# Kernel tuning notes

Measured on AMD Instinct MI355X. Metric: run time of the kernel, lower is better.

Reference implementation:

```python
import jax, jax.numpy as jnp
import numpy as np

B, V, H, W = 1, 88, 128, 256
P = 2                  # patch size
D = 128                # hidden_dim = embed_dim // latent_ratio = 1536 // 12
NG = 12                # n_group (== latent_ratio)
NH = 2                 # heads per attention = num_heads // latent_ratio = 24 // 12
E = NG * D             # embed_dim = 1536
HD = D // NH
SCALE = HD ** -0.5

# Static ragged group index sets derived from the variable names (sizes 7,7,7,7,7,9,9,9,9,9,17,6).
# Pressure-level vars are ordered z,q,t,u,v per level; levels [50..400]=7 levels, [50..600]=9 levels.
_off = {'z': 0, 'q': 1, 't': 2, 'u': 3, 'v': 4}
GROUPS = []
for name in ['u1', 'v1', 't1', 'q1', 'z1', 'u2', 'v2', 't2', 'q2', 'z2', 'surf', 'const']:
    if name[-1] in '12':
        nl = 7 if name[-1] == '1' else 9
        GROUPS.append(np.array([5 * li + _off[name[0]] for li in range(nl)]))
    elif name == 'surf':
        GROUPS.append(np.arange(65, 82))   # 17 surface vars
    else:
        GROUPS.append(np.arange(82, 88))   # 6 constant vars


def setup_inputs() -> dict:
    key = jax.random.key(0)
    ks = jax.random.split(key, 16)
    return {
        "x": jax.random.normal(ks[0], (B, V, H, W), jnp.float32),
        # per-variable conv patch-embed weights, flattened to (V, P*P, D)
        "conv_w": jax.random.normal(ks[1], (V, P * P, D), jnp.float32) * 0.05,
        "conv_b": jax.random.normal(ks[2], (V, D), jnp.float32) * 0.02,
        "channel_embed": jax.random.normal(ks[3], (1, V, D), jnp.float32) * 0.02,
        "channel_query": jax.random.uniform(ks[4], (1, NG, D), jnp.float32) * 0.2,
        # 12 distinct MultiheadAttention modules: packed in_proj (3D, D) + out_proj
        "grp_in_w": jax.random.normal(ks[5], (NG, 3 * D, D), jnp.float32) * 0.05,
        "grp_in_b": jax.random.normal(ks[6], (NG, 3 * D), jnp.float32) * 0.02,
        "grp_out_w": jax.random.normal(ks[7], (NG, D, D), jnp.float32) * 0.05,
        "grp_out_b": jax.random.normal(ks[8], (NG, D), jnp.float32) * 0.02,
        "ens_query": jax.random.uniform(ks[9], (1, NG, D), jnp.float32) * 0.2,
        "ens_in_w": jax.random.normal(ks[10], (3 * D, D), jnp.float32) * 0.05,
        "ens_in_b": jax.random.normal(ks[11], (3 * D,), jnp.float32) * 0.02,
        "ens_out_w": jax.random.normal(ks[12], (D, D), jnp.float32) * 0.05,
        "ens_out_b": jax.random.normal(ks[13], (D,), jnp.float32) * 0.02,
        "ln_gamma": jnp.ones((E,), jnp.float32),
        "ln_beta": jnp.zeros((E,), jnp.float32),
    }


def reference(x, conv_w, conv_b, channel_embed, channel_query,
              grp_in_w, grp_in_b, grp_out_w, grp_out_b,
              ens_query, ens_in_w, ens_in_b, ens_out_w, ens_out_b,
              ln_gamma, ln_beta):
    b, v, h, w = x.shape
    hp, wp = h // P, w // P
    L = hp * wp
    # non-overlapping stride-P conv with 1 input channel == patchify + per-variable matmul
    patches = x.reshape(b, v, hp, P, wp, P).transpose(0, 1, 2, 4, 3, 5).reshape(b, v, L, P * P)
    xe = jnp.einsum('bvlp,vpd->bvld', patches, conv_w) + conv_b[None, :, None, :]
    xe = xe + channel_embed[:, :, None, :]                 # (B, V, L, D)
    xn = xe.transpose(0, 2, 1, 3).reshape(b * L, v, D)     # (N, V, D), N = B*L

    outs = []
    for i, ids in enumerate(GROUPS):                       # 12 fixed, structurally distinct groups
        kv = xn[:, ids, :]                                 # (N, g, D), ragged g
        Wq, Wk, Wv = grp_in_w[i, :D], grp_in_w[i, D:2 * D], grp_in_w[i, 2 * D:]
        bq, bk, bv = grp_in_b[i, :D], grp_in_b[i, D:2 * D], grp_in_b[i, 2 * D:]
        q = (channel_query[0, i] @ Wq.T + bq).reshape(NH, HD)
        k = (kv @ Wk.T + bk).reshape(-1, len(ids), NH, HD)
        vv = (kv @ Wv.T + bv).reshape(-1, len(ids), NH, HD)
        a = jax.nn.softmax(jnp.einsum('hd,nghd->nhg', q, k) * SCALE, axis=-1)
        o = jnp.einsum('nhg,nghd->nhd', a, vv).reshape(-1, D)
        outs.append(o @ grp_out_w[i].T + grp_out_b[i])
    out = jnp.stack(outs, axis=1)                          # (N, 12, D)

    Wq, Wk, Wv = ens_in_w[:D], ens_in_w[D:2 * D], ens_in_w[2 * D:]
    bq, bk, bv = ens_in_b[:D], ens_in_b[D:2 * D], ens_in_b[2 * D:]
    q = (ens_query[0] @ Wq.T + bq).reshape(NG, NH, HD)     # 12 ensemble query tokens
    k = (out @ Wk.T + bk).reshape(-1, NG, NH, HD)
    vv = (out @ Wv.T + bv).reshape(-1, NG, NH, HD)
    a = jax.nn.softmax(jnp.einsum('thd,nshd->nhts', q, k) * SCALE, axis=-1)
    r = jnp.einsum('nhts,nshd->nthd', a, vv).reshape(-1, NG, D)
    r = (r @ ens_out_w.T + ens_out_b).reshape(b, L, E)     # (B, L, embed_dim)

    mu = r.mean(axis=-1, keepdims=True)
    var = r.var(axis=-1, keepdims=True)
    return (r - mu) * jax.lax.rsqrt(var + 1e-5) * ln_gamma + ln_beta
```

## Files before the change

kernel.cpp:

```cpp
#include <hip/hip_runtime.h>


typedef __attribute__((ext_vector_type(8))) short short8;
typedef __attribute__((ext_vector_type(4))) float f32x4;

__constant__ int GOFF[13] = {0,7,14,21,28,35,44,53,62,71,80,97,103};
__constant__ int K5A[12]  = {35,35,35,35,35,45,45,45,45,45,85,30};
__constant__ int SLOTS3[12] = {3,3,3,3,3,3,3,3,3,3,6,2};
__constant__ int FOFFA[12] = {0,3,6,9,12,15,18,21,24,27,30,36};
__constant__ int GSLOT[103] = {
  3,8,13,18,23,28,33,
  4,9,14,19,24,29,34,
  2,7,12,17,22,27,32,
  1,6,11,16,21,26,31,
  0,5,10,15,20,25,30,
  3,8,13,18,23,28,33,38,43,
  4,9,14,19,24,29,34,39,44,
  2,7,12,17,22,27,32,37,42,
  1,6,11,16,21,26,31,36,41,
  0,5,10,15,20,25,30,35,40,
  45,46,47,48,49,50,51,52,53,54,55,56,57,58,59,60,61,
  62,63,64,65,66,67};
__constant__ int GIDX[103] = {
  0,0,0,0,0,0,0, 1,1,1,1,1,1,1, 2,2,2,2,2,2,2, 3,3,3,3,3,3,3, 4,4,4,4,4,4,4,
  5,5,5,5,5,5,5,5,5, 6,6,6,6,6,6,6,6,6, 7,7,7,7,7,7,7,7,7, 8,8,8,8,8,8,8,8,8,
  9,9,9,9,9,9,9,9,9,
  10,10,10,10,10,10,10,10,10,10,10,10,10,10,10,10,10,
  11,11,11,11,11,11};
__constant__ int TGI[38] = {0,0,0,1,1,1,2,2,2,3,3,3,4,4,4,5,5,5,6,6,6,7,7,7,
                            8,8,8,9,9,9,10,10,10,10,10,10,11,11};
__constant__ int TNT[38] = {0,1,2,0,1,2,0,1,2,0,1,2,0,1,2,0,1,2,0,1,2,0,1,2,
                            0,1,2,0,1,2,0,1,2,3,4,5,0,1};

constexpr int cSLOTS[12] = {3,3,3,3,3,3,3,3,3,3,6,2};
constexpr int cFOFFA[12] = {0,3,6,9,12,15,18,21,24,27,30,36};
constexpr int cK5[12]    = {35,35,35,35,35,45,45,45,45,45,85,30};
constexpr int cGOFFC[12] = {0,7,14,21,28,35,44,53,62,71,80,97};
constexpr int cC0[12]    = {3,4,2,1,0,3,4,2,1,0,45,62};
constexpr int cSTP[12]   = {5,5,5,5,5,5,5,5,5,5,1,1};

#define QK_GRP 0
#define QK_ENS 3072
#define QB_GRP 6144
#define QB_ENS 6176
#define CGRP   6208
#define CENS   7744
#define CWQ_BYTE   43776
#define MPL_BYTE   50432
#define CW2_BYTE   836864
#define MEB_BYTE   1623296
#define QKEB_BYTE  1688832
#define FWS_BYTE   1697024

__device__ __forceinline__ float bf2f(unsigned short s) {
  return __uint_as_float(((unsigned)s) << 16);
}
__device__ __forceinline__ unsigned short f2bf(float f) {
  unsigned u = __float_as_uint(f);
  u += 0x7fffu + ((u >> 16) & 1u);
  return (unsigned short)(u >> 16);
}

__global__ void hwe_p1(const float* __restrict__ giw, const float* __restrict__ gib,
                       const float* __restrict__ gow, const float* __restrict__ gob,
                       const float* __restrict__ cq,  const float* __restrict__ eq,
                       const float* __restrict__ eiw, const float* __restrict__ eib,
                       const float* __restrict__ eow, const float* __restrict__ eob,
                       const float* __restrict__ cw,  const float* __restrict__ cb,
                       const float* __restrict__ ce,
                       float* __restrict__ wsf, unsigned short* __restrict__ MA,
                       unsigned short* __restrict__ CW2,
                       unsigned short* __restrict__ MeB, unsigned short* __restrict__ Fws) {
  int blk = blockIdx.x, tid = threadIdx.x;
  int wave = tid >> 6, lane = tid & 63;
  if (blk < 48) {
    __shared__ float qf[64];
    bool ens = blk >= 24;
    int bi = ens ? blk - 24 : blk;
    int i = bi >> 1, h = bi & 1;
    const float* W  = ens ? eiw : giw + i*49152;
    const float* bv = ens ? eib : gib + i*384;
    const float* qv = ens ? eq + i*128 : cq + i*128;
    for (int it = 0; it < 16; ++it) {
      int dp = it*4 + wave;
      const float* wrow = W + (h*64 + dp)*128;
      float acc = wrow[lane]*qv[lane] + wrow[lane+64]*qv[lane+64];
#pragma unroll
      for (int off = 32; off > 0; off >>= 1) acc += __shfl_down(acc, off);
      if (lane == 0) qf[dp] = acc + bv[h*64 + dp];
    }
    __syncthreads();
    if (tid < 128) {
      int e = tid;
      const float* Wk = W + (128 + h*64)*128 + e;
      float a0=0.f,a1=0.f,a2=0.f,a3=0.f;
      for (int dp = 0; dp < 64; dp += 4) {
        a0 += qf[dp+0] * Wk[(dp+0)*128];
        a1 += qf[dp+1] * Wk[(dp+1)*128];
        a2 += qf[dp+2] * Wk[(dp+2)*128];
        a3 += qf[dp+3] * Wk[(dp+3)*128];
      }
      wsf[(ens ? QK_ENS : QK_GRP) + bi*128 + e] = (a0+a1)+(a2+a3);
    }
    if (wave == 3) {
      float acc = qf[lane] * bv[128 + h*64 + lane];
#pragma unroll
      for (int off = 32; off > 0; off >>= 1) acc += __shfl_down(acc, off);
      if (lane == 0) wsf[(ens ? QB_ENS : QB_GRP) + bi] = acc;
    }
  } else if (blk < 1584) {
    int b2 = blk - 48;
    int gi = b2 >> 7, r = b2 & 127;
    int ep = tid, h = ep >> 7, e = ep & 127;
    const float* wo = gow + gi*16384 + r*128 + h*64;
    const float* wv = giw + gi*49152 + (256 + h*64)*128 + e;
    float a0=0.f,a1=0.f,a2=0.f,a3=0.f;
    for (int hd = 0; hd < 64; hd += 4) {
      a0 += wo[hd+0] * wv[(hd+0)*128];
      a1 += wo[hd+1] * wv[(hd+1)*128];
      a2 += wo[hd+2] * wv[(hd+2)*128];
      a3 += wo[hd+3] * wv[(hd+3)*128];
    }
    float acc = (a0+a1)+(a2+a3);
    int mt = r >> 4, lr = r & 15, kt = e >> 5, q = (e >> 3) & 3, j = e & 7;
    MA[(((gi*2 + h)*8 + mt)*4 + kt)*512 + (q*16 + lr)*8 + j] = f2bf(acc);
  } else if (blk < 1712) {
    int f2 = (blk - 1584)*256 + tid;
    int r = f2 >> 8, ep = f2 & 255;
    int h = ep >> 7, e = ep & 127;
    const float* wo = eow + r*128 + h*64;
    const float* wv = eiw + (256 + h*64)*128 + e;
    float a0=0.f,a1=0.f,a2=0.f,a3=0.f;
    for (int hd = 0; hd < 64; hd += 4) {
      a0 += wo[hd+0] * wv[(hd+0)*128];
      a1 += wo[hd+1] * wv[(hd+1)*128];
      a2 += wo[hd+2] * wv[(hd+2)*128];
      a3 += wo[hd+3] * wv[(hd+3)*128];
    }
    float acc = (a0+a1)+(a2+a3);
    int mt = r >> 4, lr = r & 15, kt = ep >> 5, q = (ep >> 3) & 3, j = ep & 7;
    MeB[((mt*8 + kt)*64 + (q*16 + lr))*8 + j] = f2bf(acc);
  } else if (blk < 2096) {
    int id = (blk - 1712)*4 + wave;
    int i = id >> 7, d = id & 127;
    const float* wrow = gow + i*16384 + d*128;
    const float* bvv = gib + i*384 + 256;
    float acc = wrow[lane]*bvv[lane] + wrow[lane+64]*bvv[lane+64];
#pragma unroll
    for (int off = 32; off > 0; off >>= 1) acc += __shfl_down(acc, off);
    if (lane == 0) wsf[CGRP + id] = acc + gob[i*128 + d];
  } else if (blk < 2128) {
    int d = (blk - 2096)*4 + wave;
    const float* wrow = eow + d*128;
    const float* bvv = eib + 256;
    float acc = wrow[lane]*bvv[lane] + wrow[lane+64]*bvv[lane+64];
#pragma unroll
    for (int off = 32; off > 0; off >>= 1) acc += __shfl_down(acc, off);
    if (lane == 0) wsf[CENS + d] = acc + eob[d];
  } else if (blk < 2166) {
    int tile = blk - 2128;
    int gi = TGI[tile], nt = TNT[tile];
    int kt = tid >> 6;
    int l15b = tid & 15, quadb = (tid >> 4) & 3;
    int k = nt*16 + l15b;
    int e = kt*32 + quadb*8;
    unsigned short vv[8];
    if (k < K5A[gi]) {
      int q = (k*205) >> 10;
      int pp = k - q*5;
      int s = GSLOT[GOFF[gi] + q];
      int v = (s < 45) ? s : s + 20;
      if (pp < 4) {
        const float* src = cw + (v*4 + pp)*128 + e;
#pragma unroll
        for (int j = 0; j < 8; ++j) vv[j] = f2bf(src[j]);
      } else {
        const float* b1 = cb + v*128 + e;
        const float* c1 = ce + v*128 + e;
#pragma unroll
        for (int j = 0; j < 8; ++j) vv[j] = f2bf(b1[j] + c1[j]);
      }
    } else {
#pragma unroll
      for (int j = 0; j < 8; ++j) vv[j] = 0;
    }
    unsigned short* dst = CW2 + (tile*4 + kt)*512 + (tid & 63)*8;
#pragma unroll
    for (int j = 0; j < 8; ++j) dst[j] = vv[j];
  } else {
    int idx = (blk - 2166)*256 + tid;
    if (idx < 19456) ((uint4*)Fws)[idx] = (uint4){0,0,0,0};
  }
}

__global__ void hwe_p2(const float* __restrict__ cw, const float* __restrict__ cb,
                       const float* __restrict__ ce,
                       const unsigned short* __restrict__ MA,
                       const unsigned short* __restrict__ CW2,
                       const float* __restrict__ wsf,
                       unsigned short* __restrict__ Fws,
                       unsigned short* __restrict__ qkeB, float* __restrict__ cwq) {
  int blk = blockIdx.x, tid = threadIdx.x;
  int wave = tid >> 6, lane = tid & 63;
  int quad = lane >> 4, l15 = lane & 15;
  if (blk < 192) {
    int gi = blk >> 4, h = (blk >> 3) & 1, mt = blk & 7;
    int K5 = K5A[gi], S = SLOTS3[gi];
    const unsigned short* MAp = MA + (((gi*2 + h)*8 + mt)*4)*512 + lane*8;
    short8 a[4];
#pragma unroll
    for (int kt = 0; kt < 4; ++kt)
      a[kt] = *(const short8*)(MAp + kt*512);
    for (int nt = wave; nt < S; nt += 4) {
      const unsigned short* Bp = CW2 + (FOFFA[gi] + nt)*2048 + lane*8;
      f32x4 acc = {0.f,0.f,0.f,0.f};
#pragma unroll
      for (int kt = 0; kt < 4; ++kt) {
        short8 b = *(const short8*)(Bp + kt*512);
        acc = __builtin_amdgcn_mfma_f32_16x16x32_bf16(a[kt], b, acc, 0, 0, 0);
      }
      int k = nt*16 + l15;
      if (k < K5) {
        int kpp = h*K5 + k;
        int base = (FOFFA[gi]*8 + mt*S + (kpp >> 5))*512
                 + ((kpp >> 3) & 3)*128 + (kpp & 7);
#pragma unroll
        for (int reg = 0; reg < 4; ++reg) {
          int rr = quad*4 + reg;
          Fws[base + rr*8] = f2bf(acc[reg]);
        }
      }
    }
  } else if (blk < 208) {
    int f4 = (blk - 192)*256 + tid;
    int ln = (f4 >> 3) & 63, j = f4 & 7;
    int th = ((f4 >> 11) & 1)*16 + (ln & 15);
    int kt = (f4 >> 9) & 3;
    float val = (th < 24) ? wsf[QK_ENS + th*128 + kt*32 + (ln >> 4)*8 + j] : 0.f;
    qkeB[f4] = f2bf(val);
  } else {
    int wid = (blk - 208)*4 + wave;
    if (wid < 206) {
      int gg = wid >> 1, h = wid & 1;
      int gi = GIDX[gg];
      int s = GSLOT[gg];
      int v = (s < 45) ? s : s + 20;
      const float* qk = wsf + QK_GRP + (gi*2 + h)*128;
      float q0 = qk[lane], q1 = qk[lane + 64];
      float a[5];
#pragma unroll
      for (int pp = 0; pp < 4; ++pp)
        a[pp] = cw[(v*4 + pp)*128 + lane]*q0 + cw[(v*4 + pp)*128 + lane + 64]*q1;
      a[4] = (cb[v*128 + lane] + ce[v*128 + lane])*q0 +
             (cb[v*128 + lane + 64] + ce[v*128 + lane + 64])*q1;
#pragma unroll
      for (int off = 32; off > 0; off >>= 1)
#pragma unroll
        for (int kk = 0; kk < 5; ++kk) a[kk] += __shfl_down(a[kk], off);
      if (lane == 0) {
        float* o = cwq + (gg*2 + h)*8;
        o[0] = a[0]*0.125f; o[1] = a[1]*0.125f; o[2] = a[2]*0.125f; o[3] = a[3]*0.125f;
        o[4] = (a[4] + wsf[QB_GRP + gi*2 + h]) * 0.125f;
      }
    }
  }
}

__global__ __launch_bounds__(256, 4) void hwe_main(
    const float* __restrict__ x,
    const float* __restrict__ lgam, const float* __restrict__ lbet,
    const float* __restrict__ wsf,  const float* __restrict__ cwq,
    const unsigned short* __restrict__ Fws, const unsigned short* __restrict__ MeB,
    const unsigned short* __restrict__ qkeB,
    float* __restrict__ out) {
  __shared__ __align__(16) unsigned char smem[40576];
  unsigned short* xpB   = (unsigned short*)(smem);
  unsigned short* scb   = (unsigned short*)(smem + 4352);
  unsigned short* wpAll = (unsigned short*)(smem + 7680);
  unsigned short* Gl    = (unsigned short*)(smem);
  unsigned short* sce2  = (unsigned short*)(smem + 10240);
  unsigned short* outg2 = (unsigned short*)(smem + 15872);
  float*          stats = (float*)(smem + 40448);

  const int tid  = threadIdx.x;
  const int wave = tid >> 6;
  const int lane = tid & 63;
  const int quad = lane >> 4;
  const int l15  = lane & 15;

  const int hi   = blockIdx.x >> 4;
  const int wib  = (blockIdx.x & 15) << 3;
  const int nbase = hi*128 + wib;

  for (int idx = tid; idx < 1088; idx += 256) {
    int c2 = idx & 7, r = (idx >> 3) & 1, s = idx >> 4;
    int v = (s < 45) ? s : s + 20;
    const float2 xv = *(const float2*)(x + (v*128 + 2*hi + r)*256 + 2*wib + c2*2);
    unsigned pk = (unsigned)f2bf(xv.x) | ((unsigned)f2bf(xv.y) << 16);
    *(unsigned*)(xpB + (c2*68 + s)*4 + r*2) = pk;
  }
  __syncthreads();

  for (int idx = tid; idx < 1648; idx += 256) {
    int h = idx & 1, p = (idx >> 1) & 7, gg = idx >> 4;
    int s = GSLOT[gg];
    const float* c = cwq + (gg*2 + h)*8;
    const unsigned short* xr = xpB + (p*68 + s)*4;
    float acc = c[4] + bf2f(xr[0])*c[0] + bf2f(xr[1])*c[1]
                     + bf2f(xr[2])*c[2] + bf2f(xr[3])*c[3];
    scb[(p*2 + h)*104 + gg] = f2bf(acc);
  }
  __syncthreads();

  if (tid < 192) {
    int gi = tid % 12, h = (tid / 12) & 1, p = tid / 24;
    int go = GOFF[gi], G = GOFF[gi+1] - go;
    unsigned short* row = scb + (p*2 + h)*104 + go;
    float ev[17];
    float m = -1e30f;
#pragma unroll
    for (int g = 0; g < 17; ++g) {
      ev[g] = (g < G) ? bf2f(row[g]) : -1e30f;
      m = fmaxf(m, ev[g]);
    }
    float ssum = 0.f;
#pragma unroll
    for (int g = 0; g < 17; ++g) {
      float e = __expf(ev[g] - m);
      ev[g] = e;
      if (g < G) ssum += e;
    }
    float inv = 1.f / ssum;
#pragma unroll
    for (int g = 0; g < 17; ++g)
      if (g < G) row[g] = f2bf(ev[g] * inv);
  }
  __syncthreads();

  {
    short8 fA[6], fB[6];
    float4 cgA, cgB;
    auto fws_issue = [&](int gi, int mh, short8 (&buf)[6], float4& cg) {
      int S = cSLOTS[gi];
      int mt = mh*4 + wave;
      const unsigned short* fp = Fws + (cFOFFA[gi]*8 + mt*S)*512 + lane*8;
#pragma unroll
      for (int kt = 0; kt < 6; ++kt)
        if (kt < S) buf[kt] = *(const short8*)(fp + kt*512);
      cg = *(const float4*)(wsf + CGRP + gi*128 + mt*16 + quad*4);
    };
    auto fws_compute = [&](int gi, int mh, int lbase, short8 (&buf)[6],
                           const float4& cg) {
      int S = cSLOTS[gi];
      int mt = mh*4 + wave;
      f32x4 acc = {0.f,0.f,0.f,0.f};
#pragma unroll
      for (int kt = 0; kt < 6; ++kt)
        if (kt < S) {
          short8 b = *(const short8*)(wpAll + (lbase + kt)*512 + lane*8);
          acc = __builtin_amdgcn_mfma_f32_16x16x32_bf16(buf[kt], b, acc, 0, 0, 0);
        }
      if (l15 < 8) {
        int p = l15;
        int rb = mt*16 + quad*4;
        unsigned short t0 = f2bf(acc[0] + cg.x);
        unsigned short t1 = f2bf(acc[1] + cg.y);
        unsigned short t2 = f2bf(acc[2] + cg.z);
        unsigned short t3 = f2bf(acc[3] + cg.w);
        uint2 w;
        w.x = (unsigned)t0 | ((unsigned)t1 << 16);
        w.y = (unsigned)t2 | ((unsigned)t3 << 16);
        int row = gi*8 + p;
        int ch = (rb >> 3) ^ ((gi ^ p) & 7);
        *(uint2*)(outg2 + row*128 + ch*8 + (rb & 7)) = w;
      }
    };

    fws_issue(0, 0, fA, cgA);

#pragma unroll
    for (int ph = 0; ph < 6; ++ph) {
      const int g0 = 2*ph;
      const int S0 = cSLOTS[g0];
      const int nsl = S0 + cSLOTS[g0+1];

      {
        const int nposs = nsl * 512;
        for (int pos = tid*4; pos < nposs; pos += 1024) {
          int pf = (pos >> 3) & 15;
          uint2 w2 = {0u, 0u};
          if (pf < 8) {
            int ls = pos >> 9;
            int qd = (pos >> 7) & 3;
            int j0 = pos & 7;
            int p  = pf;
            bool gsel = (ls >= S0);
            int lsl   = gsel ? ls - S0 : ls;
            int K5    = gsel ? cK5[g0+1]    : cK5[g0];
            int goffB = gsel ? cGOFFC[g0+1] : cGOFFC[g0];
            int c0    = gsel ? cC0[g0+1]    : cC0[g0];
            int stp   = gsel ? cSTP[g0+1]   : cSTP[g0];
            int kbase = lsl*32 + qd*8 + j0;
            unsigned short vv[4];
#pragma unroll
            for (int jj = 0; jj < 4; ++jj) {
              int kpp = kbase + jj;
              int h = (kpp >= K5) ? 1 : 0;
              int k = kpp - (h ? K5 : 0);
              int q = (k*205) >> 10;
              int pp = k - q*5;
              int gg = goffB + q;
              int s = c0 + q*stp;
              float a  = bf2f(scb[(p*2 + h)*104 + gg]);
              float xv = bf2f(xpB[(p*68 + s)*4 + pp]);
              float val = (pp < 4) ? a * xv : a;
              if (kpp >= 2*K5) val = 0.f;
              vv[jj] = f2bf(val);
            }
            w2.x = (unsigned)vv[0] | ((unsigned)vv[1] << 16);
            w2.y = (unsigned)vv[2] | ((unsigned)vv[3] << 16);
          }
          *(uint2*)(wpAll + pos) = w2;
        }
      }
      __syncthreads();

      fws_issue(g0+0, 1, fB, cgB);
      fws_compute(g0+0, 0, 0,  fA, cgA);
      fws_issue(g0+1, 0, fA, cgA);
      fws_compute(g0+0, 1, 0,  fB, cgB);
      fws_issue(g0+1, 1, fB, cgB);
      fws_compute(g0+1, 0, S0, fA, cgA);
      if (ph < 5) fws_issue(g0+2, 0, fA, cgA);
      fws_compute(g0+1, 1, S0, fB, cgB);
      __syncthreads();
    }
  }

  float cens0[4], cens1[4];
  {
    float4 c0 = *(const float4*)(wsf + CENS + (wave*2 + 0)*16 + quad*4);
    float4 c1 = *(const float4*)(wsf + CENS + (wave*2 + 1)*16 + quad*4);
    cens0[0]=c0.x; cens0[1]=c0.y; cens0[2]=c0.z; cens0[3]=c0.w;
    cens1[0]=c1.x; cens1[1]=c1.y; cens1[2]=c1.z; cens1[3]=c1.w;
  }
  short8 meAr[16];
#pragma unroll
  for (int mi = 0; mi < 2; ++mi)
#pragma unroll
    for (int h = 0; h < 2; ++h)
#pragma unroll
      for (int kt = 0; kt < 4; ++kt)
        meAr[(mi*2 + h)*4 + kt] =
          *(const short8*)(MeB + (((wave*2 + mi)*8 + h*4 + kt)*64 + lane)*8);

#pragma unroll
  for (int ti = 0; ti < 3; ++ti) {
    int T = wave*3 + ti;
    int mtp = T >> 1, ntp = T & 1;
    int rowA = mtp*16 + l15;
    int sx = ((rowA >> 3) ^ rowA) & 7;
    f32x4 acc = {0.f,0.f,0.f,0.f};
#pragma unroll
    for (int kt = 0; kt < 4; ++kt) {
      short8 a = *(const short8*)(outg2 + rowA*128 + (((kt*4 + quad) ^ sx) << 3));
      short8 b = *(const short8*)(qkeB + ((ntp*4 + kt)*64 + lane)*8);
      acc = __builtin_amdgcn_mfma_f32_16x16x32_bf16(a, b, acc, 0, 0, 0);
    }
    int th = ntp*16 + l15;
    if (th < 24) {
      float qb = wsf[QB_ENS + th];
#pragma unroll
      for (int reg = 0; reg < 4; ++reg) {
        int rowE = mtp*16 + quad*4 + reg;
        sce2[((rowE & 7)*24 + th)*12 + (rowE >> 3)] = f2bf((acc[reg] + qb) * 0.125f);
      }
    }
  }
  __syncthreads();

  if (tid < 192) {
    unsigned short* row = sce2 + tid*12;
    float ev[12];
    float m = -1e30f;
#pragma unroll
    for (int s = 0; s < 12; ++s) { ev[s] = bf2f(row[s]); m = fmaxf(m, ev[s]); }
    float ssum = 0.f;
#pragma unroll
    for (int s = 0; s < 12; ++s) { float e = __expf(ev[s] - m); ev[s] = e; ssum += e; }
    float inv = 1.f / ssum;
#pragma unroll
    for (int s = 0; s < 12; ++s) row[s] = f2bf(ev[s] * inv);
  }
  __syncthreads();

  for (int pp2 = 0; pp2 < 4; ++pp2) {
    f32x4 g[2][2][2];
#pragma unroll
    for (int lp = 0; lp < 2; ++lp)
#pragma unroll
      for (int mi = 0; mi < 2; ++mi)
#pragma unroll
        for (int h = 0; h < 2; ++h) g[lp][mi][h] = (f32x4){0.f,0.f,0.f,0.f};
#pragma unroll
    for (int lp = 0; lp < 2; ++lp) {
      int p = pp2*2 + lp;
      int brow = (l15 < 12) ? (l15*8 + p) : 0;
      int sx = ((brow >> 3) ^ brow) & 7;
#pragma unroll
      for (int h = 0; h < 2; ++h) {
#pragma unroll
        for (int kt = 0; kt < 4; ++kt) {
          short8 b = *(const short8*)(outg2 + brow*128 + (((kt*4 + quad) ^ sx) << 3));
          if (l15 >= 12) b = (short8){0,0,0,0,0,0,0,0};
          g[lp][0][h] = __builtin_amdgcn_mfma_f32_16x16x32_bf16(
              meAr[(0*2 + h)*4 + kt], b, g[lp][0][h], 0, 0, 0);
          g[lp][1][h] = __builtin_amdgcn_mfma_f32_16x16x32_bf16(
              meAr[(1*2 + h)*4 + kt], b, g[lp][1][h], 0, 0, 0);
        }
      }
    }

    f32x4 rr[2][2];
    float s1[2] = {0.f, 0.f}, s2[2] = {0.f, 0.f};
#pragma unroll
    for (int lp = 0; lp < 2; ++lp) {
      int p = pp2*2 + lp;
#pragma unroll
      for (int mi = 0; mi < 2; ++mi)
#pragma unroll
        for (int h = 0; h < 2; ++h)
#pragma unroll
          for (int reg = 0; reg < 4; ++reg) {
            int r = (wave*2 + mi)*16 + quad*4 + reg;
            Gl[r*40 + h*16 + l15] = f2bf(g[lp][mi][h][reg]);
          }
      short8 af0 = *(const short8*)(Gl + ((wave*2 + 0)*16 + l15)*40 + quad*8);
      short8 af1 = *(const short8*)(Gl + ((wave*2 + 1)*16 + l15)*40 + quad*8);
      union { short8 s8; uint4 u4; } bu;
      {
        const unsigned short* sp = sce2 + (p*24 + l15*2 + (quad >> 1))*12 + (quad & 1)*8;
        uint2 lo = *(const uint2*)(sp);
        uint2 hi2 = *(const uint2*)(sp + 4);
        if (quad & 1) { hi2.x = 0u; hi2.y = 0u; }
        if (l15 >= 12) { lo.x = 0u; lo.y = 0u; hi2.x = 0u; hi2.y = 0u; }
        bu.u4.x = lo.x; bu.u4.y = lo.y; bu.u4.z = hi2.x; bu.u4.w = hi2.y;
      }
#pragma unroll
      for (int mi = 0; mi < 2; ++mi) {
        f32x4 acc = {0.f,0.f,0.f,0.f};
        acc = __builtin_amdgcn_mfma_f32_16x16x32_bf16(mi ? af1 : af0, bu.s8,
                                                      acc, 0, 0, 0);
#pragma unroll
        for (int reg = 0; reg < 4; ++reg)
          acc[reg] += (mi ? cens1[reg] : cens0[reg]);
        rr[lp][mi] = acc;
        if (l15 < 12) {
#pragma unroll
          for (int reg = 0; reg < 4; ++reg) {
            float v = acc[reg];
            s1[lp] += v; s2[lp] += v*v;
          }
        }
      }
    }
#pragma unroll
    for (int off = 32; off > 0; off >>= 1) {
#pragma unroll
      for (int lp = 0; lp < 2; ++lp) {
        s1[lp] += __shfl_xor(s1[lp], off);
        s2[lp] += __shfl_xor(s2[lp], off);
      }
    }
    int sb = (pp2 & 1) << 4;
    if (lane == 0) {
#pragma unroll
      for (int lp = 0; lp < 2; ++lp) {
        stats[sb + lp*4 + wave] = s1[lp];
        stats[sb + 8 + lp*4 + wave] = s2[lp];
      }
    }
    __syncthreads();
#pragma unroll
    for (int lp = 0; lp < 2; ++lp) {
      float t1 = stats[sb+lp*4+0] + stats[sb+lp*4+1] + stats[sb+lp*4+2] + stats[sb+lp*4+3];
      float t2 = stats[sb+8+lp*4+0] + stats[sb+8+lp*4+1] + stats[sb+8+lp*4+2] + stats[sb+8+lp*4+3];
      float mean = t1 * (1.f/1536.f);
      float var  = t2 * (1.f/1536.f) - mean*mean;
      float rstd = rsqrtf(var + 1e-5f);
      if (l15 < 12) {
        long nrow = (long)(nbase + pp2*2 + lp) * 1536;
#pragma unroll
        for (int mi = 0; mi < 2; ++mi) {
          int rb = (wave*2 + mi)*16 + quad*4;
          int j = l15*128 + rb;
          float4 gm = *(const float4*)(lgam + j);
          float4 bt = *(const float4*)(lbet + j);
          float4 o;
          o.x = (rr[lp][mi][0] - mean)*rstd*gm.x + bt.x;
          o.y = (rr[lp][mi][1] - mean)*rstd*gm.y + bt.y;
          o.z = (rr[lp][mi][2] - mean)*rstd*gm.z + bt.z;
          o.w = (rr[lp][mi][3] - mean)*rstd*gm.w + bt.w;
          *(float4*)(out + nrow + j) = o;
        }
      }
    }
  }
}

extern "C" void kernel_launch(void* const* d_in, const int* in_sizes, int n_in,
                              void* d_out, int out_size, void* d_ws, size_t ws_size,
                              hipStream_t stream) {
  const float* x   = (const float*)d_in[0];
  const float* cw  = (const float*)d_in[1];
  const float* cb  = (const float*)d_in[2];
  const float* ce  = (const float*)d_in[3];
  const float* cq  = (const float*)d_in[4];
  const float* giw = (const float*)d_in[5];
  const float* gib = (const float*)d_in[6];
  const float* gow = (const float*)d_in[7];
  const float* gob = (const float*)d_in[8];
  const float* eq  = (const float*)d_in[9];
  const float* eiw = (const float*)d_in[10];
  const float* eib = (const float*)d_in[11];
  const float* eow = (const float*)d_in[12];
  const float* eob = (const float*)d_in[13];
  const float* lg  = (const float*)d_in[14];
  const float* lb  = (const float*)d_in[15];

  float* wsf = (float*)d_ws;
  float* cwq = (float*)((char*)d_ws + CWQ_BYTE);
  unsigned short* MA   = (unsigned short*)((char*)d_ws + MPL_BYTE);
  unsigned short* CW2  = (unsigned short*)((char*)d_ws + CW2_BYTE);
  unsigned short* MeB  = (unsigned short*)((char*)d_ws + MEB_BYTE);
  unsigned short* qkeB = (unsigned short*)((char*)d_ws + QKEB_BYTE);
  unsigned short* Fws  = (unsigned short*)((char*)d_ws + FWS_BYTE);

  hwe_p1<<<2242, 256, 0, stream>>>(giw, gib, gow, gob, cq, eq, eiw, eib, eow, eob,
                                   cw, cb, ce, wsf, MA, CW2, MeB, Fws);
  hwe_p2<<<260, 256, 0, stream>>>(cw, cb, ce, MA, CW2, wsf, Fws, qkeB, cwq);
  hwe_main<<<1024, 256, 0, stream>>>(x, lg, lb, wsf, cwq, Fws, MeB, qkeB,
                                     (float*)d_out);
}
```

Measured before the change: 182.1 us.

## Split main kernel into group-attention and ensemble kernels staging through output buffer

Splits the fused main kernel into two kernels. The first computes the per-group attention outputs and writes them as bf16 into the second half of each block's slice of the output buffer. The second kernel reads them back and runs the ensemble attention and layernorm. Each kernel needs much less LDS and declares 8 blocks per SM, so occupancy should rise. The cost is an extra launch and a global-memory round trip, and the second kernel must read its staged data before overwriting that same region of the output.

```diff
diff --git a/kernel.cpp b/kernel.cpp
--- a/kernel.cpp
+++ b/kernel.cpp
@@ -34,10 +34,6 @@
 
 constexpr int cSLOTS[12] = {3,3,3,3,3,3,3,3,3,3,6,2};
 constexpr int cFOFFA[12] = {0,3,6,9,12,15,18,21,24,27,30,36};
-constexpr int cK5[12]    = {35,35,35,35,35,45,45,45,45,45,85,30};
-constexpr int cGOFFC[12] = {0,7,14,21,28,35,44,53,62,71,80,97};
-constexpr int cC0[12]    = {3,4,2,1,0,3,4,2,1,0,45,62};
-constexpr int cSTP[12]   = {5,5,5,5,5,5,5,5,5,5,1,1};
 
 #define QK_GRP 0
 #define QK_ENS 3072
@@ -266,21 +262,15 @@
   }
 }
 
-__global__ __launch_bounds__(256, 4) void hwe_main(
+__global__ __launch_bounds__(256, 8) void hwe_mAB(
     const float* __restrict__ x,
-    const float* __restrict__ lgam, const float* __restrict__ lbet,
     const float* __restrict__ wsf,  const float* __restrict__ cwq,
-    const unsigned short* __restrict__ Fws, const unsigned short* __restrict__ MeB,
-    const unsigned short* __restrict__ qkeB,
+    const unsigned short* __restrict__ Fws,
     float* __restrict__ out) {
-  __shared__ __align__(16) unsigned char smem[40576];
+  __shared__ __align__(16) unsigned char smem[15872];
   unsigned short* xpB   = (unsigned short*)(smem);
   unsigned short* scb   = (unsigned short*)(smem + 4352);
   unsigned short* wpAll = (unsigned short*)(smem + 7680);
-  unsigned short* Gl    = (unsigned short*)(smem);
-  unsigned short* sce2  = (unsigned short*)(smem + 10240);
-  unsigned short* outg2 = (unsigned short*)(smem + 15872);
-  float*          stats = (float*)(smem + 40448);
 
   const int tid  = threadIdx.x;
   const int wave = tid >> 6;
@@ -290,7 +280,8 @@
 
   const int hi   = blockIdx.x >> 4;
   const int wib  = (blockIdx.x & 15) << 3;
-  const int nbase = hi*128 + wib;
+  unsigned short* outG =
+      (unsigned short*)((char*)out + (size_t)blockIdx.x*49152 + 24576);
 
   for (int idx = tid; idx < 1088; idx += 256) {
     int c2 = idx & 7, r = (idx >> 3) & 1, s = idx >> 4;
@@ -370,9 +361,7 @@
         uint2 w;
         w.x = (unsigned)t0 | ((unsigned)t1 << 16);
         w.y = (unsigned)t2 | ((unsigned)t3 << 16);
-        int row = gi*8 + p;
-        int ch = (rb >> 3) ^ ((gi ^ p) & 7);
-        *(uint2*)(outg2 + row*128 + ch*8 + (rb & 7)) = w;
+        *(uint2*)(outG + (p*12 + gi)*128 + rb) = w;
       }
     };
 
@@ -396,10 +385,9 @@
             int p  = pf;
             bool gsel = (ls >= S0);
             int lsl   = gsel ? ls - S0 : ls;
-            int K5    = gsel ? cK5[g0+1]    : cK5[g0];
-            int goffB = gsel ? cGOFFC[g0+1] : cGOFFC[g0];
-            int c0    = gsel ? cC0[g0+1]    : cC0[g0];
-            int stp   = gsel ? cSTP[g0+1]   : cSTP[g0];
+            int gi    = g0 + (gsel ? 1 : 0);
+            int K5    = K5A[gi];
+            int goffB = GOFF[gi];
             int kbase = lsl*32 + qd*8 + j0;
             unsigned short vv[4];
 #pragma unroll
@@ -410,9 +398,8 @@
               int q = (k*205) >> 10;
               int pp = k - q*5;
               int gg = goffB + q;
-              int s = c0 + q*stp;
               float a  = bf2f(scb[(p*2 + h)*104 + gg]);
-              float xv = bf2f(xpB[(p*68 + s)*4 + pp]);
+              float xv = bf2f(xpB[(p*68 + GSLOT[gg])*4 + pp]);
               float val = (pp < 4) ? a * xv : a;
               if (kpp >= 2*K5) val = 0.f;
               vv[jj] = f2bf(val);
@@ -436,6 +423,30 @@
       __syncthreads();
     }
   }
+}
+
+__global__ __launch_bounds__(256, 8) void hwe_mC(
+    const float* __restrict__ lgam, const float* __restrict__ lbet,
+    const float* __restrict__ wsf,
+    const unsigned short* __restrict__ MeB,
+    const unsigned short* __restrict__ qkeB,
+    float* __restrict__ out) {
+  __shared__ __align__(16) unsigned char smem[14976];
+  unsigned short* Gl    = (unsigned short*)(smem);
+  unsigned short* sce2  = (unsigned short*)(smem + 10240);
+  float*          stats = (float*)(smem + 14848);
+
+  const int tid  = threadIdx.x;
+  const int wave = tid >> 6;
+  const int lane = tid & 63;
+  const int quad = lane >> 4;
+  const int l15  = lane & 15;
+
+  const int hi   = blockIdx.x >> 4;
+  const int wib  = (blockIdx.x & 15) << 3;
+  const int nbase = hi*128 + wib;
+  const unsigned short* outG =
+      (const unsigned short*)((const char*)out + (size_t)blockIdx.x*49152 + 24576);
 
   float cens0[4], cens1[4];
   {
@@ -459,11 +470,11 @@
     int T = wave*3 + ti;
     int mtp = T >> 1, ntp = T & 1;
     int rowA = mtp*16 + l15;
-    int sx = ((rowA >> 3) ^ rowA) & 7;
+    const unsigned short* ap = outG + ((rowA & 7)*12 + (rowA >> 3))*128;
     f32x4 acc = {0.f,0.f,0.f,0.f};
 #pragma unroll
     for (int kt = 0; kt < 4; ++kt) {
-      short8 a = *(const short8*)(outg2 + rowA*128 + (((kt*4 + quad) ^ sx) << 3));
+      short8 a = *(const short8*)(ap + kt*32 + quad*8);
       short8 b = *(const short8*)(qkeB + ((ntp*4 + kt)*64 + lane)*8);
       acc = __builtin_amdgcn_mfma_f32_16x16x32_bf16(a, b, acc, 0, 0, 0);
     }
@@ -505,13 +516,13 @@
 #pragma unroll
     for (int lp = 0; lp < 2; ++lp) {
       int p = pp2*2 + lp;
-      int brow = (l15 < 12) ? (l15*8 + p) : 0;
-      int sx = ((brow >> 3) ^ brow) & 7;
+      int gi_ = (l15 < 12) ? l15 : 0;
+      const unsigned short* bp = outG + (p*12 + gi_)*128;
 #pragma unroll
       for (int h = 0; h < 2; ++h) {
 #pragma unroll
         for (int kt = 0; kt < 4; ++kt) {
-          short8 b = *(const short8*)(outg2 + brow*128 + (((kt*4 + quad) ^ sx) << 3));
+          short8 b = *(const short8*)(bp + kt*32 + quad*8);
           if (l15 >= 12) b = (short8){0,0,0,0,0,0,0,0};
           g[lp][0][h] = __builtin_amdgcn_mfma_f32_16x16x32_bf16(
               meAr[(0*2 + h)*4 + kt], b, g[lp][0][h], 0, 0, 0);
@@ -639,6 +650,6 @@
   hwe_p1<<<2242, 256, 0, stream>>>(giw, gib, gow, gob, cq, eq, eiw, eib, eow, eob,
                                    cw, cb, ce, wsf, MA, CW2, MeB, Fws);
   hwe_p2<<<260, 256, 0, stream>>>(cw, cb, ce, MA, CW2, wsf, Fws, qkeB, cwq);
-  hwe_main<<<1024, 256, 0, stream>>>(x, lg, lb, wsf, cwq, Fws, MeB, qkeB,
-                                     (float*)d_out);
+  hwe_mAB<<<1024, 256, 0, stream>>>(x, wsf, cwq, Fws, (float*)d_out);
+  hwe_mC<<<1024, 256, 0, stream>>>(lg, lb, wsf, MeB, qkeB, (float*)d_out);
 }
```

Measured after the change: 296.0 us. 62.5% more time.
